# Optimization experiments

Hardware: AMD Instinct MI355X
Metric: run time of the kernel (lower is better)

Reference implementation:

```python
import jax, jax.numpy as jnp
import numpy as np
import math

HIDDEN = 512
NUM_HEADS = 8
HEAD_DIM = HIDDEN // NUM_HEADS  # 64
B, S = 64, 128


def setup_inputs() -> dict:
    key = jax.random.key(0)
    ks = jax.random.split(key, 16)
    sc_h = 1.0 / math.sqrt(HIDDEN)
    sc_d = 1.0 / math.sqrt(HEAD_DIM)
    return {
        "hidden_states": jax.random.normal(ks[0], (B, S, HIDDEN), jnp.float32),
        "attention_mask": jnp.zeros((B, 1, S, S), jnp.float32),
        "structure_matrix": jax.random.normal(ks[1], (B, S, S, HEAD_DIM), jnp.float32),
        # projections stored [in, out]
        "Wq": jax.random.normal(ks[2], (HIDDEN, HIDDEN), jnp.float32) * sc_h,
        "bq": jnp.zeros((HIDDEN,), jnp.float32),
        "Wk": jax.random.normal(ks[3], (HIDDEN, HIDDEN), jnp.float32) * sc_h,
        "bk": jnp.zeros((HIDDEN,), jnp.float32),
        "Wv": jax.random.normal(ks[4], (HIDDEN, HIDDEN), jnp.float32) * sc_h,
        "bv": jnp.zeros((HIDDEN,), jnp.float32),
        "Wsq": jax.random.normal(ks[5], (HEAD_DIM, HEAD_DIM), jnp.float32) * sc_d,
        "bsq": jnp.zeros((HEAD_DIM,), jnp.float32),
        "Wsk": jax.random.normal(ks[6], (HEAD_DIM, HEAD_DIM), jnp.float32) * sc_d,
        "bsk": jnp.zeros((HEAD_DIM,), jnp.float32),
        "Wsv": jax.random.normal(ks[7], (HEAD_DIM, HEAD_DIM), jnp.float32) * sc_d,
        "bsv": jnp.zeros((HEAD_DIM,), jnp.float32),
    }


def _heads(x):
    b, s, _ = x.shape
    return x.reshape(b, s, NUM_HEADS, HEAD_DIM).transpose(0, 2, 1, 3)  # [B,H,S,D]


def reference(hidden_states, attention_mask, structure_matrix,
              Wq, bq, Wk, bk, Wv, bv, Wsq, bsq, Wsk, bsk, Wsv, bsv):
    # projections
    q = _heads(hidden_states @ Wq + bq)  # [B,H,S,D]
    k = _heads(hidden_states @ Wk + bk)
    v = _heads(hidden_states @ Wv + bv)
    sq = structure_matrix @ Wsq + bsq    # [B,S,S,D] (i=key idx, j=query idx)
    sk = structure_matrix @ Wsk + bsk
    sv = structure_matrix @ Wsv + bsv
    # scores[b,h,i,j] = sum_d (k_i + sk_ij)(q_j + sq_ij), expanded to avoid 5D tensor
    scores = (
        jnp.einsum('bhid,bhjd->bhij', k, q)
        + jnp.einsum('bhid,bijd->bhij', k, sq)
        + jnp.einsum('bhjd,bijd->bhij', q, sk)
        + jnp.einsum('bijd,bijd->bij', sk, sq)[:, None]
    ) / math.sqrt(HEAD_DIM)
    scores = scores + attention_mask
    p = jax.nn.relu(scores)
    # note: torch code sums (p + 1e-12) over last dim, i.e. denom = sum(p) + S*1e-12
    p = p / jnp.sum(p + 1e-12, axis=-1, keepdims=True)
    # out[b,h,i,d] = sum_j p_ij * (v_j + sv_ij)
    ctx = (jnp.einsum('bhij,bhjd->bhid', p, v)
           + jnp.einsum('bhij,bijd->bhid', p, sv))
    b = ctx.shape[0]
    return ctx.transpose(0, 2, 1, 3).reshape(b, S, HIDDEN)
```

## Files before the change

kernel.cpp:

```cpp
#include <hip/hip_runtime.h>

#define B_  64
#define S_  128
#define H_  8
#define D_  64
#define HID 512

typedef short short8 __attribute__((ext_vector_type(8)));
typedef float f32x4 __attribute__((ext_vector_type(4)));

__device__ __forceinline__ float bf2f(unsigned short h) {
    union { unsigned int u; float f; } v; v.u = (unsigned int)h << 16; return v.f;
}
__device__ __forceinline__ unsigned short f2bf(float f) {
    union { float f; unsigned int u; } v; v.f = f;
    unsigned int r = v.u + 0x7fffu + ((v.u >> 16) & 1u);
    return (unsigned short)(r >> 16);
}

__global__ __launch_bounds__(256) void wtrans(const float* __restrict__ s0,
                                              const float* __restrict__ s1,
                                              const float* __restrict__ s2,
                                              unsigned short* __restrict__ dst0, int dim)
{
    const float* srcs[3] = {s0, s1, s2};
    const float* src = srcs[blockIdx.z];
    unsigned short* dst = dst0 + (size_t)blockIdx.z * dim * dim;
    __shared__ float tile[32][33];
    const int tx = threadIdx.x & 31, ty = threadIdx.x >> 5;
    const int k0 = blockIdx.x * 32, n0 = blockIdx.y * 32;
    #pragma unroll
    for (int r = 0; r < 4; ++r) {
        int row = ty + r * 8;
        tile[row][tx] = src[(size_t)(k0 + row) * dim + n0 + tx];
    }
    __syncthreads();
    #pragma unroll
    for (int r = 0; r < 4; ++r) {
        int row = ty + r * 8;
        dst[(size_t)(n0 + row) * dim + k0 + tx] = f2bf(tile[tx][row]);
    }
}

__global__ __launch_bounds__(256) void qkv_mfma(
    const float* __restrict__ hidden,
    const unsigned short* __restrict__ wt,
    const float* __restrict__ bq, const float* __restrict__ bk, const float* __restrict__ bv,
    unsigned short* __restrict__ Qb,
    unsigned short* __restrict__ Kb,
    unsigned short* __restrict__ Vb)
{
    const int z = blockIdx.z;
    const unsigned short* W = wt + (size_t)z * HID * HID;
    const float* bias = (z == 0) ? bq : (z == 1) ? bk : bv;
    const int bm = blockIdx.y * 128, bn = blockIdx.x * 128;
    const int t = threadIdx.x, lane = t & 63, w = t >> 6, grp = lane >> 4, l15 = lane & 15;

    __shared__ unsigned short a_s[128 * 72];
    __shared__ unsigned short b_s[128 * 72];

    f32x4 acc[2][8];
    #pragma unroll
    for (int i = 0; i < 2; ++i)
        #pragma unroll
        for (int j = 0; j < 8; ++j) acc[i][j] = (f32x4){0.f, 0.f, 0.f, 0.f};

    for (int k0 = 0; k0 < HID; k0 += 64) {
        #pragma unroll
        for (int it = 0; it < 8; ++it) {
            int idx = t + it * 256;
            int row = idx >> 4, c = idx & 15;
            float4 v4 = *reinterpret_cast<const float4*>(&hidden[(size_t)(bm + row) * HID + k0 + c * 4]);
            ushort4 o = {f2bf(v4.x), f2bf(v4.y), f2bf(v4.z), f2bf(v4.w)};
            *reinterpret_cast<ushort4*>(&a_s[row * 72 + c * 4]) = o;
        }
        #pragma unroll
        for (int it = 0; it < 4; ++it) {
            int idx = t + it * 256;
            int row = idx >> 3, c = idx & 7;
            *reinterpret_cast<short8*>(&b_s[row * 72 + c * 8]) =
                *reinterpret_cast<const short8*>(&W[(size_t)(bn + row) * HID + k0 + c * 8]);
        }
        __syncthreads();
        short8 af[2][2];
        #pragma unroll
        for (int mt = 0; mt < 2; ++mt)
            #pragma unroll
            for (int kk = 0; kk < 2; ++kk)
                af[mt][kk] = *reinterpret_cast<const short8*>(&a_s[(w * 32 + mt * 16 + l15) * 72 + kk * 32 + grp * 8]);
        #pragma unroll
        for (int nt = 0; nt < 8; ++nt) {
            short8 b0 = *reinterpret_cast<const short8*>(&b_s[(nt * 16 + l15) * 72 + grp * 8]);
            short8 b1 = *reinterpret_cast<const short8*>(&b_s[(nt * 16 + l15) * 72 + 32 + grp * 8]);
            #pragma unroll
            for (int mt = 0; mt < 2; ++mt) {
                acc[mt][nt] = __builtin_amdgcn_mfma_f32_16x16x32_bf16(af[mt][0], b0, acc[mt][nt], 0, 0, 0);
                acc[mt][nt] = __builtin_amdgcn_mfma_f32_16x16x32_bf16(af[mt][1], b1, acc[mt][nt], 0, 0, 0);
            }
        }
        __syncthreads();
    }
    unsigned short* dstqk = (z == 0) ? Qb : Kb;
    #pragma unroll
    for (int nt = 0; nt < 8; ++nt) {
        int col = bn + nt * 16 + l15;
        float bval = bias[col];
        #pragma unroll
        for (int mt = 0; mt < 2; ++mt) {
            #pragma unroll
            for (int r = 0; r < 4; ++r) {
                int row = bm + w * 32 + mt * 16 + grp * 4 + r;
                unsigned short val = f2bf(acc[mt][nt][r] + bval);
                if (z == 2) {
                    Vb[(size_t)row * HID + col] = val;
                } else {
                    int bb = row >> 7, jj = row & 127, hh = col >> 6, dd = col & 63;
                    dstqk[(((size_t)bb * H_ + hh) * S_ + jj) * D_ + dd] = val;
                }
            }
        }
    }
}

__global__ __launch_bounds__(256) void kq_gemm(
    const unsigned short* __restrict__ Kb, const unsigned short* __restrict__ Qb,
    float* __restrict__ sc0)
{
    const int bh = blockIdx.x;
    const int t = threadIdx.x, lane = t & 63, w = t >> 6, grp = lane >> 4, l15 = lane & 15;
    const unsigned short* Kp = Kb + (size_t)bh * S_ * D_;
    const unsigned short* Qp = Qb + (size_t)bh * S_ * D_;
    float* outp = sc0 + (size_t)bh * S_ * S_;
    short8 af[2][2];
    #pragma unroll
    for (int mt = 0; mt < 2; ++mt)
        #pragma unroll
        for (int kk = 0; kk < 2; ++kk)
            af[mt][kk] = *reinterpret_cast<const short8*>(&Kp[(size_t)(w * 32 + mt * 16 + l15) * D_ + kk * 32 + grp * 8]);
    #pragma unroll
    for (int nt = 0; nt < 8; ++nt) {
        short8 b0 = *reinterpret_cast<const short8*>(&Qp[(size_t)(nt * 16 + l15) * D_ + grp * 8]);
        short8 b1 = *reinterpret_cast<const short8*>(&Qp[(size_t)(nt * 16 + l15) * D_ + 32 + grp * 8]);
        #pragma unroll
        for (int mt = 0; mt < 2; ++mt) {
            f32x4 a = {0.f, 0.f, 0.f, 0.f};
            a = __builtin_amdgcn_mfma_f32_16x16x32_bf16(af[mt][0], b0, a, 0, 0, 0);
            a = __builtin_amdgcn_mfma_f32_16x16x32_bf16(af[mt][1], b1, a, 0, 0, 0);
            #pragma unroll
            for (int r = 0; r < 4; ++r)
                outp[(size_t)(w * 32 + mt * 16 + grp * 4 + r) * S_ + nt * 16 + l15] = a[r];
        }
    }
}

__global__ __launch_bounds__(256) void attn2(
    const unsigned short* __restrict__ Qb, const unsigned short* __restrict__ Kb,
    const unsigned short* __restrict__ Vb,
    const float* __restrict__ sc0,
    const float* __restrict__ st, const float* __restrict__ mask,
    const unsigned short* __restrict__ wtS,
    const float* __restrict__ bsq, const float* __restrict__ bsk, const float* __restrict__ bsv,
    float* __restrict__ out)
{
    const int i = blockIdx.x, b = blockIdx.y;
    const int t = threadIdx.x, lane = t & 63, w = t >> 6, grp = lane >> 4, l15 = lane & 15;

    __shared__ __align__(16) unsigned char smem[76096];
    unsigned short* st_s = (unsigned short*)smem;
    float*          scf  = (float*)smem;
    unsigned short* sq_s = (unsigned short*)(smem + 18432);
    unsigned short* sk_s = (unsigned short*)(smem + 36864);
    unsigned short* sv_s = (unsigned short*)(smem + 55296);
    unsigned short* k_s  = (unsigned short*)(smem + 73728);
    float*          rsp  = (float*)(smem + 76032);

    {
        const float* stp = st + ((size_t)b * S_ + i) * S_ * D_;
        #pragma unroll
        for (int it = 0; it < 8; ++it) {
            int idx = t + it * 256;
            int row = idx >> 4, c = idx & 15;
            float4 v4 = *reinterpret_cast<const float4*>(stp + (size_t)idx * 4);
            ushort4 o = {f2bf(v4.x), f2bf(v4.y), f2bf(v4.z), f2bf(v4.w)};
            *reinterpret_cast<ushort4*>(&st_s[row * 72 + c * 4]) = o;
        }
        if (t < 64) {
            int h = t >> 3, c = t & 7;
            *reinterpret_cast<short8*>(&k_s[h * 72 + c * 8]) =
                *reinterpret_cast<const short8*>(&Kb[(((size_t)b * H_ + h) * S_ + i) * D_ + c * 8]);
        } else if (t < 128) {
            int h = 8 + ((t - 64) >> 3), c = t & 7;
            short8 zz = {0, 0, 0, 0, 0, 0, 0, 0};
            *reinterpret_cast<short8*>(&k_s[h * 72 + c * 8]) = zz;
        }
    }
    __syncthreads();

    {
        short8 af[2][2];
        #pragma unroll
        for (int mt = 0; mt < 2; ++mt)
            #pragma unroll
            for (int kk = 0; kk < 2; ++kk)
                af[mt][kk] = *reinterpret_cast<const short8*>(&st_s[(w * 32 + mt * 16 + l15) * 72 + kk * 32 + grp * 8]);
        const float* bss[3] = {bsq, bsk, bsv};
        unsigned short* outs[3] = {sq_s, sk_s, sv_s};
        #pragma unroll
        for (int p = 0; p < 3; ++p) {
            const unsigned short* Wp = wtS + (size_t)p * 64 * 64;
            #pragma unroll
            for (int nt = 0; nt < 4; ++nt) {
                short8 b0 = *reinterpret_cast<const short8*>(&Wp[(size_t)(nt * 16 + l15) * 64 + grp * 8]);
                short8 b1 = *reinterpret_cast<const short8*>(&Wp[(size_t)(nt * 16 + l15) * 64 + 32 + grp * 8]);
                float bval = bss[p][nt * 16 + l15];
                #pragma unroll
                for (int mt = 0; mt < 2; ++mt) {
                    f32x4 a = {0.f, 0.f, 0.f, 0.f};
                    a = __builtin_amdgcn_mfma_f32_16x16x32_bf16(af[mt][0], b0, a, 0, 0, 0);
                    a = __builtin_amdgcn_mfma_f32_16x16x32_bf16(af[mt][1], b1, a, 0, 0, 0);
                    #pragma unroll
                    for (int r = 0; r < 4; ++r)
                        outs[p][(w * 32 + mt * 16 + grp * 4 + r) * 72 + nt * 16 + l15] = f2bf(a[r] + bval);
                }
            }
        }
    }
    __syncthreads();

    {
        short8 ka0 = *reinterpret_cast<const short8*>(&k_s[l15 * 72 + grp * 8]);
        short8 ka1 = *reinterpret_cast<const short8*>(&k_s[l15 * 72 + 32 + grp * 8]);
        #pragma unroll
        for (int nt = 0; nt < 2; ++nt) {
            int j0 = w * 32 + nt * 16;
            short8 b0 = *reinterpret_cast<const short8*>(&sq_s[(j0 + l15) * 72 + grp * 8]);
            short8 b1 = *reinterpret_cast<const short8*>(&sq_s[(j0 + l15) * 72 + 32 + grp * 8]);
            f32x4 a = {0.f, 0.f, 0.f, 0.f};
            a = __builtin_amdgcn_mfma_f32_16x16x32_bf16(ka0, b0, a, 0, 0, 0);
            a = __builtin_amdgcn_mfma_f32_16x16x32_bf16(ka1, b1, a, 0, 0, 0);
            if (grp < 2) {
                #pragma unroll
                for (int r = 0; r < 4; ++r)
                    scf[(grp * 4 + r) * 128 + j0 + l15] = a[r];
            }
        }
    }
    __syncthreads();

    const int jj = (w & 1) * 64 + lane;
    const int hg = w >> 1;
    {
        const unsigned short* skr = &sk_s[jj * 72];
        const unsigned short* sqr = &sq_s[jj * 72];
        const unsigned short* qp = Qb + (((size_t)b * H_ + hg * 4) * S_ + jj) * D_;
        float a0 = 0.f, a1 = 0.f, a2 = 0.f, a3 = 0.f, ss = 0.f;
        #pragma unroll
        for (int c = 0; c < 8; ++c) {
            short8 sk8 = *reinterpret_cast<const short8*>(&skr[c * 8]);
            short8 sq8 = *reinterpret_cast<const short8*>(&sqr[c * 8]);
            short8 q0 = *reinterpret_cast<const short8*>(&qp[c * 8]);
            short8 q1 = *reinterpret_cast<const short8*>(&qp[S_ * D_ + c * 8]);
            short8 q2 = *reinterpret_cast<const short8*>(&qp[2 * S_ * D_ + c * 8]);
            short8 q3 = *reinterpret_cast<const short8*>(&qp[3 * S_ * D_ + c * 8]);
            #pragma unroll
            for (int e = 0; e < 8; ++e) {
                float skf = bf2f((unsigned short)sk8[e]);
                float sqf = bf2f((unsigned short)sq8[e]);
                a0 += bf2f((unsigned short)q0[e]) * skf;
                a1 += bf2f((unsigned short)q1[e]) * skf;
                a2 += bf2f((unsigned short)q2[e]) * skf;
                a3 += bf2f((unsigned short)q3[e]) * skf;
                ss += skf * sqf;
            }
        }
        float mv = mask[((size_t)b * S_ + i) * S_ + jj];
        const float* s0p = sc0 + (((size_t)b * H_ + hg * 4) * S_ + i) * S_ + jj;
        float qsk[4] = {a0, a1, a2, a3};
        float pv[4];
        #pragma unroll
        for (int hh = 0; hh < 4; ++hh) {
            int h = hg * 4 + hh;
            float kqv = s0p[(size_t)hh * S_ * S_];
            float ksqv = scf[h * 128 + jj];
            float s = (kqv + ksqv + qsk[hh] + ss) * 0.125f + mv;
            pv[hh] = fmaxf(s, 0.f);
        }
        #pragma unroll
        for (int hh = 0; hh < 4; ++hh) {
            scf[(hg * 4 + hh) * 128 + jj] = pv[hh];
            float r = pv[hh];
            #pragma unroll
            for (int off = 1; off < 64; off <<= 1) r += __shfl_xor(r, off);
            if (lane == 0) rsp[w * 4 + hh] = r;
        }
    }
    __syncthreads();

    {
        const int hc = t >> 6, dc = t & 63;
        const int h0 = hc, h1 = hc + 4;
        float den0 = rsp[((h0 >> 2) * 2) * 4 + (h0 & 3)] + rsp[((h0 >> 2) * 2 + 1) * 4 + (h0 & 3)] + 1.28e-10f;
        float den1 = rsp[((h1 >> 2) * 2) * 4 + (h1 & 3)] + rsp[((h1 >> 2) * 2 + 1) * 4 + (h1 & 3)] + 1.28e-10f;
        const unsigned short* vp = Vb + (size_t)b * S_ * HID;
        float c0 = 0.f, c1 = 0.f;
        #pragma unroll 4
        for (int j = 0; j < S_; ++j) {
            float p0 = scf[h0 * 128 + j];
            float p1 = scf[h1 * 128 + j];
            float svv = bf2f(sv_s[j * 72 + dc]);
            float v0 = bf2f(vp[(size_t)j * HID + h0 * 64 + dc]);
            float v1 = bf2f(vp[(size_t)j * HID + h1 * 64 + dc]);
            c0 += p0 * (v0 + svv);
            c1 += p1 * (v1 + svv);
        }
        float* orow = out + ((size_t)b * S_ + i) * HID;
        orow[t]       = c0 / den0;
        orow[t + 256] = c1 / den1;
    }
}

extern "C" void kernel_launch(void* const* d_in, const int* in_sizes, int n_in,
                              void* d_out, int out_size, void* d_ws, size_t ws_size,
                              hipStream_t stream) {
    const float* hidden = (const float*)d_in[0];
    const float* mask   = (const float*)d_in[1];
    const float* st     = (const float*)d_in[2];
    const float* Wq  = (const float*)d_in[3];
    const float* bq  = (const float*)d_in[4];
    const float* Wk  = (const float*)d_in[5];
    const float* bk  = (const float*)d_in[6];
    const float* Wv  = (const float*)d_in[7];
    const float* bv  = (const float*)d_in[8];
    const float* Wsq = (const float*)d_in[9];
    const float* bsq = (const float*)d_in[10];
    const float* Wsk = (const float*)d_in[11];
    const float* bsk = (const float*)d_in[12];
    const float* Wsv = (const float*)d_in[13];
    const float* bsv = (const float*)d_in[14];
    float* out = (float*)d_out;

    unsigned char* ws = (unsigned char*)d_ws;
    unsigned short* wtB = (unsigned short*)(ws);
    unsigned short* wtS = (unsigned short*)(ws + 1572864);
    unsigned short* Qb  = (unsigned short*)(ws + 1597440);
    unsigned short* Kb  = (unsigned short*)(ws + 9986048);
    unsigned short* Vb  = (unsigned short*)(ws + 18374656);
    float*          sc0 = (float*)(ws + 26763264);

    wtrans<<<dim3(16, 16, 3), 256, 0, stream>>>(Wq, Wk, Wv, wtB, 512);
    wtrans<<<dim3(2, 2, 3), 256, 0, stream>>>(Wsq, Wsk, Wsv, wtS, 64);
    qkv_mfma<<<dim3(4, 64, 3), 256, 0, stream>>>(hidden, wtB, bq, bk, bv, Qb, Kb, Vb);
    kq_gemm<<<dim3(512), 256, 0, stream>>>(Kb, Qb, sc0);
    attn2<<<dim3(S_, B_), 256, 0, stream>>>(Qb, Kb, Vb, sc0, st, mask, wtS, bsq, bsk, bsv, out);
}
```

Before: 470.3 us.

## Rewrite attention kernel with multi-row blocks, prefetch, swizzled LDS and MFMA PV

Replaces the per-row attention kernel with one that processes 8 query rows per block, register-prefetching the next structure-matrix slice while computing the current one. LDS layouts drop padding in favor of XOR swizzles, block indices are remapped for locality, and the P·(V+SV) product moves from scalar loops to MFMA using a transposed V layout emitted by the QKV GEMM. The K·Q scores and probabilities are stored as bf16, and packed hardware bf16 conversion is used. This cuts global traffic and scalar FMA work but lowers precision and serializes 8 rows per block, reducing the number of blocks available for parallelism.

```diff
diff --git a/kernel.cpp b/kernel.cpp
--- a/kernel.cpp
+++ b/kernel.cpp
@@ -5,6 +5,7 @@
 #define H_  8
 #define D_  64
 #define HID 512
+#define G_  8
 
 typedef short short8 __attribute__((ext_vector_type(8)));
 typedef float f32x4 __attribute__((ext_vector_type(4)));
@@ -16,6 +17,11 @@
     union { float f; unsigned int u; } v; v.f = f;
     unsigned int r = v.u + 0x7fffu + ((v.u >> 16) & 1u);
     return (unsigned short)(r >> 16);
+}
+__device__ __forceinline__ unsigned int cvt_pk_bf16(float lo, float hi) {
+    unsigned int r;
+    asm("v_cvt_pk_bf16_f32 %0, %1, %2" : "=v"(r) : "v"(lo), "v"(hi));
+    return r;
 }
 
 __global__ __launch_bounds__(256) void wtrans(const float* __restrict__ s0,
@@ -48,7 +54,7 @@
     const float* __restrict__ bq, const float* __restrict__ bk, const float* __restrict__ bv,
     unsigned short* __restrict__ Qb,
     unsigned short* __restrict__ Kb,
-    unsigned short* __restrict__ Vb)
+    unsigned short* __restrict__ VT)
 {
     const int z = blockIdx.z;
     const unsigned short* W = wt + (size_t)z * HID * HID;
@@ -71,8 +77,9 @@
             int idx = t + it * 256;
             int row = idx >> 4, c = idx & 15;
             float4 v4 = *reinterpret_cast<const float4*>(&hidden[(size_t)(bm + row) * HID + k0 + c * 4]);
-            ushort4 o = {f2bf(v4.x), f2bf(v4.y), f2bf(v4.z), f2bf(v4.w)};
-            *reinterpret_cast<ushort4*>(&a_s[row * 72 + c * 4]) = o;
+            unsigned int lo = cvt_pk_bf16(v4.x, v4.y);
+            unsigned int hi = cvt_pk_bf16(v4.z, v4.w);
+            *reinterpret_cast<uint2*>(&a_s[row * 72 + c * 4]) = make_uint2(lo, hi);
         }
         #pragma unroll
         for (int it = 0; it < 4; ++it) {
@@ -111,10 +118,10 @@
             for (int r = 0; r < 4; ++r) {
                 int row = bm + w * 32 + mt * 16 + grp * 4 + r;
                 unsigned short val = f2bf(acc[mt][nt][r] + bval);
+                int bb = row >> 7, jj = row & 127, hh = col >> 6, dd = col & 63;
                 if (z == 2) {
-                    Vb[(size_t)row * HID + col] = val;
+                    VT[(((size_t)bb * H_ + hh) * D_ + dd) * S_ + jj] = val;
                 } else {
-                    int bb = row >> 7, jj = row & 127, hh = col >> 6, dd = col & 63;
                     dstqk[(((size_t)bb * H_ + hh) * S_ + jj) * D_ + dd] = val;
                 }
             }
@@ -124,13 +131,13 @@
 
 __global__ __launch_bounds__(256) void kq_gemm(
     const unsigned short* __restrict__ Kb, const unsigned short* __restrict__ Qb,
-    float* __restrict__ sc0)
+    unsigned short* __restrict__ sc0)
 {
     const int bh = blockIdx.x;
     const int t = threadIdx.x, lane = t & 63, w = t >> 6, grp = lane >> 4, l15 = lane & 15;
     const unsigned short* Kp = Kb + (size_t)bh * S_ * D_;
     const unsigned short* Qp = Qb + (size_t)bh * S_ * D_;
-    float* outp = sc0 + (size_t)bh * S_ * S_;
+    unsigned short* outp = sc0 + (size_t)bh * S_ * S_;
     short8 af[2][2];
     #pragma unroll
     for (int mt = 0; mt < 2; ++mt)
@@ -148,174 +155,215 @@
             a = __builtin_amdgcn_mfma_f32_16x16x32_bf16(af[mt][1], b1, a, 0, 0, 0);
             #pragma unroll
             for (int r = 0; r < 4; ++r)
-                outp[(size_t)(w * 32 + mt * 16 + grp * 4 + r) * S_ + nt * 16 + l15] = a[r];
-        }
-    }
-}
-
-__global__ __launch_bounds__(256) void attn2(
+                outp[(size_t)(w * 32 + mt * 16 + grp * 4 + r) * S_ + nt * 16 + l15] = f2bf(a[r]);
+        }
+    }
+}
+
+__global__ __launch_bounds__(256) void attn3(
     const unsigned short* __restrict__ Qb, const unsigned short* __restrict__ Kb,
-    const unsigned short* __restrict__ Vb,
-    const float* __restrict__ sc0,
+    const unsigned short* __restrict__ VT,
+    const unsigned short* __restrict__ sc0,
     const float* __restrict__ st, const float* __restrict__ mask,
     const unsigned short* __restrict__ wtS,
     const float* __restrict__ bsq, const float* __restrict__ bsk, const float* __restrict__ bsv,
     float* __restrict__ out)
 {
-    const int i = blockIdx.x, b = blockIdx.y;
+    const int flat = blockIdx.y * gridDim.x + blockIdx.x;
+    const int swz  = (flat & 7) * 128 + (flat >> 3);
+    const int b  = swz >> 4;
+    const int ig = swz & 15;
     const int t = threadIdx.x, lane = t & 63, w = t >> 6, grp = lane >> 4, l15 = lane & 15;
 
-    __shared__ __align__(16) unsigned char smem[76096];
-    unsigned short* st_s = (unsigned short*)smem;
-    float*          scf  = (float*)smem;
-    unsigned short* sq_s = (unsigned short*)(smem + 18432);
-    unsigned short* sk_s = (unsigned short*)(smem + 36864);
-    unsigned short* sv_s = (unsigned short*)(smem + 55296);
-    unsigned short* k_s  = (unsigned short*)(smem + 73728);
-    float*          rsp  = (float*)(smem + 76032);
-
+    __shared__ __align__(16) unsigned char smem[53312];
+    float* rsp = (float*)(smem + 53248);
+
+    const float* stbase = st + (size_t)b * S_ * S_ * D_;
+    float4 stg[8];
     {
-        const float* stp = st + ((size_t)b * S_ + i) * S_ * D_;
-        #pragma unroll
-        for (int it = 0; it < 8; ++it) {
-            int idx = t + it * 256;
-            int row = idx >> 4, c = idx & 15;
-            float4 v4 = *reinterpret_cast<const float4*>(stp + (size_t)idx * 4);
-            ushort4 o = {f2bf(v4.x), f2bf(v4.y), f2bf(v4.z), f2bf(v4.w)};
-            *reinterpret_cast<ushort4*>(&st_s[row * 72 + c * 4]) = o;
+        const float* p = stbase + (size_t)(ig * G_) * (S_ * D_);
+        #pragma unroll
+        for (int l = 0; l < 8; ++l)
+            stg[l] = *reinterpret_cast<const float4*>(p + (size_t)(t + l * 256) * 4);
+    }
+
+    for (int it = 0; it < G_; ++it) {
+        const int i = ig * G_ + it;
+
+        #pragma unroll
+        for (int l = 0; l < 8; ++l) {
+            const int idx = t + l * 256;
+            const int row = idx >> 4, c = idx & 15;
+            unsigned int lo = cvt_pk_bf16(stg[l].x, stg[l].y);
+            unsigned int hi = cvt_pk_bf16(stg[l].z, stg[l].w);
+            *reinterpret_cast<uint2*>((char*)smem + row * 128 + ((((c >> 1) ^ (row & 7)) << 4)) + 8 * (c & 1))
+                = make_uint2(lo, hi);
+        }
+        __syncthreads();
+
+        short8 af[2][2];
+        #pragma unroll
+        for (int mt = 0; mt < 2; ++mt) {
+            const int row = w * 32 + mt * 16 + l15, rs = row & 7;
+            af[mt][0] = *reinterpret_cast<const short8*>((const char*)smem + row * 128 + ((grp ^ rs) << 4));
+            af[mt][1] = *reinterpret_cast<const short8*>((const char*)smem + row * 128 + (((4 + grp) ^ rs) << 4));
+        }
+        __syncthreads();
+
+        if (it + 1 < G_) {
+            const float* nxt = stbase + (size_t)(i + 1) * (S_ * D_);
+            #pragma unroll
+            for (int l = 0; l < 8; ++l)
+                stg[l] = *reinterpret_cast<const float4*>(nxt + (size_t)(t + l * 256) * 4);
         }
         if (t < 64) {
-            int h = t >> 3, c = t & 7;
-            *reinterpret_cast<short8*>(&k_s[h * 72 + c * 8]) =
-                *reinterpret_cast<const short8*>(&Kb[(((size_t)b * H_ + h) * S_ + i) * D_ + c * 8]);
-        } else if (t < 128) {
-            int h = 8 + ((t - 64) >> 3), c = t & 7;
-            short8 zz = {0, 0, 0, 0, 0, 0, 0, 0};
-            *reinterpret_cast<short8*>(&k_s[h * 72 + c * 8]) = zz;
-        }
-    }
-    __syncthreads();
-
-    {
-        short8 af[2][2];
-        #pragma unroll
-        for (int mt = 0; mt < 2; ++mt)
-            #pragma unroll
-            for (int kk = 0; kk < 2; ++kk)
-                af[mt][kk] = *reinterpret_cast<const short8*>(&st_s[(w * 32 + mt * 16 + l15) * 72 + kk * 32 + grp * 8]);
-        const float* bss[3] = {bsq, bsk, bsv};
-        unsigned short* outs[3] = {sq_s, sk_s, sv_s};
-        #pragma unroll
-        for (int p = 0; p < 3; ++p) {
-            const unsigned short* Wp = wtS + (size_t)p * 64 * 64;
-            #pragma unroll
-            for (int nt = 0; nt < 4; ++nt) {
-                short8 b0 = *reinterpret_cast<const short8*>(&Wp[(size_t)(nt * 16 + l15) * 64 + grp * 8]);
-                short8 b1 = *reinterpret_cast<const short8*>(&Wp[(size_t)(nt * 16 + l15) * 64 + 32 + grp * 8]);
-                float bval = bss[p][nt * 16 + l15];
+            const int h = t >> 3, c = t & 7;
+            short8 kv = *reinterpret_cast<const short8*>(&Kb[(((size_t)b * H_ + h) * S_ + i) * D_ + c * 8]);
+            *reinterpret_cast<short8*>((char*)smem + 49152 + h * 128 + (((c ^ (h & 7)) << 4))) = kv;
+        }
+        {
+            #pragma unroll
+            for (int p = 0; p < 3; ++p) {
+                const unsigned short* Wp = wtS + p * (D_ * D_);
+                const float* bsp = (p == 0) ? bsq : (p == 1) ? bsk : bsv;
                 #pragma unroll
-                for (int mt = 0; mt < 2; ++mt) {
-                    f32x4 a = {0.f, 0.f, 0.f, 0.f};
-                    a = __builtin_amdgcn_mfma_f32_16x16x32_bf16(af[mt][0], b0, a, 0, 0, 0);
-                    a = __builtin_amdgcn_mfma_f32_16x16x32_bf16(af[mt][1], b1, a, 0, 0, 0);
+                for (int nt = 0; nt < 4; ++nt) {
+                    short8 bf0 = *reinterpret_cast<const short8*>(&Wp[(size_t)(nt * 16 + l15) * D_ + grp * 8]);
+                    short8 bf1 = *reinterpret_cast<const short8*>(&Wp[(size_t)(nt * 16 + l15) * D_ + 32 + grp * 8]);
+                    float bval = bsp[nt * 16 + l15];
+                    #pragma unroll
+                    for (int mt = 0; mt < 2; ++mt) {
+                        f32x4 a = (f32x4){0.f, 0.f, 0.f, 0.f};
+                        a = __builtin_amdgcn_mfma_f32_16x16x32_bf16(af[mt][0], bf0, a, 0, 0, 0);
+                        a = __builtin_amdgcn_mfma_f32_16x16x32_bf16(af[mt][1], bf1, a, 0, 0, 0);
+                        const int jrow = w * 32 + mt * 16 + grp * 4;
+                        if (p == 2) {
+                            const int e = nt * 16 + l15;
+                            unsigned int lo = cvt_pk_bf16(a[0] + bval, a[1] + bval);
+                            unsigned int hi = cvt_pk_bf16(a[2] + bval, a[3] + bval);
+                            const int slot = (4 * w + 2 * mt + (grp >> 1)) ^ (e & 7);
+                            *reinterpret_cast<uint2*>((char*)smem + 32768 + (e << 8) + (slot << 4) + 8 * (grp & 1))
+                                = make_uint2(lo, hi);
+                        } else {
+                            char* oB = (char*)smem + (p == 0 ? 16384 : 0);
+                            #pragma unroll
+                            for (int r = 0; r < 4; ++r) {
+                                const int row = jrow + r;
+                                const int slot = (2 * nt + (l15 >> 3)) ^ (row & 7);
+                                *reinterpret_cast<unsigned short*>(oB + row * 128 + (slot << 4) + ((2 * l15) & 15))
+                                    = f2bf(a[r] + bval);
+                            }
+                        }
+                    }
+                }
+            }
+        }
+        __syncthreads();
+
+        {
+            const char* kB = (const char*)smem + 49152;
+            const int ks = l15 & 7;
+            short8 ka0 = *reinterpret_cast<const short8*>(kB + l15 * 128 + ((grp ^ ks) << 4));
+            short8 ka1 = *reinterpret_cast<const short8*>(kB + l15 * 128 + (((4 + grp) ^ ks) << 4));
+            unsigned short* kqs = (unsigned short*)(smem + 51200);
+            const char* sqB = (const char*)smem + 16384;
+            #pragma unroll
+            for (int nt2 = 0; nt2 < 2; ++nt2) {
+                const int j0 = w * 32 + nt2 * 16;
+                const int row = j0 + l15, rs = row & 7;
+                short8 b0 = *reinterpret_cast<const short8*>(sqB + row * 128 + ((grp ^ rs) << 4));
+                short8 b1 = *reinterpret_cast<const short8*>(sqB + row * 128 + (((4 + grp) ^ rs) << 4));
+                f32x4 a = (f32x4){0.f, 0.f, 0.f, 0.f};
+                a = __builtin_amdgcn_mfma_f32_16x16x32_bf16(ka0, b0, a, 0, 0, 0);
+                a = __builtin_amdgcn_mfma_f32_16x16x32_bf16(ka1, b1, a, 0, 0, 0);
+                if (grp < 2) {
                     #pragma unroll
                     for (int r = 0; r < 4; ++r)
-                        outs[p][(w * 32 + mt * 16 + grp * 4 + r) * 72 + nt * 16 + l15] = f2bf(a[r] + bval);
+                        kqs[(grp * 4 + r) * S_ + j0 + l15] = f2bf(a[r]);
                 }
             }
         }
-    }
-    __syncthreads();
-
-    {
-        short8 ka0 = *reinterpret_cast<const short8*>(&k_s[l15 * 72 + grp * 8]);
-        short8 ka1 = *reinterpret_cast<const short8*>(&k_s[l15 * 72 + 32 + grp * 8]);
-        #pragma unroll
-        for (int nt = 0; nt < 2; ++nt) {
-            int j0 = w * 32 + nt * 16;
-            short8 b0 = *reinterpret_cast<const short8*>(&sq_s[(j0 + l15) * 72 + grp * 8]);
-            short8 b1 = *reinterpret_cast<const short8*>(&sq_s[(j0 + l15) * 72 + 32 + grp * 8]);
-            f32x4 a = {0.f, 0.f, 0.f, 0.f};
-            a = __builtin_amdgcn_mfma_f32_16x16x32_bf16(ka0, b0, a, 0, 0, 0);
-            a = __builtin_amdgcn_mfma_f32_16x16x32_bf16(ka1, b1, a, 0, 0, 0);
-            if (grp < 2) {
+        __syncthreads();
+
+        {
+            const int jj = (w & 1) * 64 + lane;
+            const int hg = w >> 1;
+            const int jsw = jj & 7;
+            const char* skB = (const char*)smem + jj * 128;
+            const char* sqB = (const char*)smem + 16384 + jj * 128;
+            const unsigned short* qp = Qb + (((size_t)b * H_ + hg * 4) * S_ + jj) * D_;
+            float a0 = 0.f, a1 = 0.f, a2 = 0.f, a3 = 0.f, ss = 0.f;
+            #pragma unroll
+            for (int c = 0; c < 8; ++c) {
+                const int off = (c ^ jsw) << 4;
+                short8 sk8 = *reinterpret_cast<const short8*>(skB + off);
+                short8 sq8 = *reinterpret_cast<const short8*>(sqB + off);
+                short8 q0 = *reinterpret_cast<const short8*>(&qp[c * 8]);
+                short8 q1 = *reinterpret_cast<const short8*>(&qp[S_ * D_ + c * 8]);
+                short8 q2 = *reinterpret_cast<const short8*>(&qp[2 * S_ * D_ + c * 8]);
+                short8 q3 = *reinterpret_cast<const short8*>(&qp[3 * S_ * D_ + c * 8]);
                 #pragma unroll
-                for (int r = 0; r < 4; ++r)
-                    scf[(grp * 4 + r) * 128 + j0 + l15] = a[r];
-            }
-        }
-    }
-    __syncthreads();
-
-    const int jj = (w & 1) * 64 + lane;
-    const int hg = w >> 1;
-    {
-        const unsigned short* skr = &sk_s[jj * 72];
-        const unsigned short* sqr = &sq_s[jj * 72];
-        const unsigned short* qp = Qb + (((size_t)b * H_ + hg * 4) * S_ + jj) * D_;
-        float a0 = 0.f, a1 = 0.f, a2 = 0.f, a3 = 0.f, ss = 0.f;
-        #pragma unroll
-        for (int c = 0; c < 8; ++c) {
-            short8 sk8 = *reinterpret_cast<const short8*>(&skr[c * 8]);
-            short8 sq8 = *reinterpret_cast<const short8*>(&sqr[c * 8]);
-            short8 q0 = *reinterpret_cast<const short8*>(&qp[c * 8]);
-            short8 q1 = *reinterpret_cast<const short8*>(&qp[S_ * D_ + c * 8]);
-            short8 q2 = *reinterpret_cast<const short8*>(&qp[2 * S_ * D_ + c * 8]);
-            short8 q3 = *reinterpret_cast<const short8*>(&qp[3 * S_ * D_ + c * 8]);
-            #pragma unroll
-            for (int e = 0; e < 8; ++e) {
-                float skf = bf2f((unsigned short)sk8[e]);
-                float sqf = bf2f((unsigned short)sq8[e]);
-                a0 += bf2f((unsigned short)q0[e]) * skf;
-                a1 += bf2f((unsigned short)q1[e]) * skf;
-                a2 += bf2f((unsigned short)q2[e]) * skf;
-                a3 += bf2f((unsigned short)q3[e]) * skf;
-                ss += skf * sqf;
-            }
-        }
-        float mv = mask[((size_t)b * S_ + i) * S_ + jj];
-        const float* s0p = sc0 + (((size_t)b * H_ + hg * 4) * S_ + i) * S_ + jj;
-        float qsk[4] = {a0, a1, a2, a3};
-        float pv[4];
-        #pragma unroll
-        for (int hh = 0; hh < 4; ++hh) {
-            int h = hg * 4 + hh;
-            float kqv = s0p[(size_t)hh * S_ * S_];
-            float ksqv = scf[h * 128 + jj];
-            float s = (kqv + ksqv + qsk[hh] + ss) * 0.125f + mv;
-            pv[hh] = fmaxf(s, 0.f);
-        }
-        #pragma unroll
-        for (int hh = 0; hh < 4; ++hh) {
-            scf[(hg * 4 + hh) * 128 + jj] = pv[hh];
-            float r = pv[hh];
-            #pragma unroll
-            for (int off = 1; off < 64; off <<= 1) r += __shfl_xor(r, off);
-            if (lane == 0) rsp[w * 4 + hh] = r;
-        }
-    }
-    __syncthreads();
-
-    {
-        const int hc = t >> 6, dc = t & 63;
-        const int h0 = hc, h1 = hc + 4;
-        float den0 = rsp[((h0 >> 2) * 2) * 4 + (h0 & 3)] + rsp[((h0 >> 2) * 2 + 1) * 4 + (h0 & 3)] + 1.28e-10f;
-        float den1 = rsp[((h1 >> 2) * 2) * 4 + (h1 & 3)] + rsp[((h1 >> 2) * 2 + 1) * 4 + (h1 & 3)] + 1.28e-10f;
-        const unsigned short* vp = Vb + (size_t)b * S_ * HID;
-        float c0 = 0.f, c1 = 0.f;
-        #pragma unroll 4
-        for (int j = 0; j < S_; ++j) {
-            float p0 = scf[h0 * 128 + j];
-            float p1 = scf[h1 * 128 + j];
-            float svv = bf2f(sv_s[j * 72 + dc]);
-            float v0 = bf2f(vp[(size_t)j * HID + h0 * 64 + dc]);
-            float v1 = bf2f(vp[(size_t)j * HID + h1 * 64 + dc]);
-            c0 += p0 * (v0 + svv);
-            c1 += p1 * (v1 + svv);
-        }
-        float* orow = out + ((size_t)b * S_ + i) * HID;
-        orow[t]       = c0 / den0;
-        orow[t + 256] = c1 / den1;
+                for (int e = 0; e < 8; ++e) {
+                    float skf = bf2f((unsigned short)sk8[e]);
+                    float sqf = bf2f((unsigned short)sq8[e]);
+                    a0 += bf2f((unsigned short)q0[e]) * skf;
+                    a1 += bf2f((unsigned short)q1[e]) * skf;
+                    a2 += bf2f((unsigned short)q2[e]) * skf;
+                    a3 += bf2f((unsigned short)q3[e]) * skf;
+                    ss += skf * sqf;
+                }
+            }
+            const float mv = mask[((size_t)b * S_ + i) * S_ + jj];
+            const unsigned short* s0p = sc0 + (((size_t)b * H_ + hg * 4) * S_ + i) * S_ + jj;
+            const unsigned short* kqs = (const unsigned short*)(smem + 51200);
+            unsigned short* pbf = (unsigned short*)(smem + 49152);
+            float qsk[4] = {a0, a1, a2, a3};
+            #pragma unroll
+            for (int hh = 0; hh < 4; ++hh) {
+                const int h = hg * 4 + hh;
+                float kqv  = bf2f(s0p[(size_t)hh * S_ * S_]);
+                float ksqv = bf2f(kqs[h * S_ + jj]);
+                float s = (kqv + ksqv + qsk[hh] + ss) * 0.125f + mv;
+                float pv = fmaxf(s, 0.f);
+                pbf[h * S_ + jj] = f2bf(pv);
+                float r = pv;
+                #pragma unroll
+                for (int o2 = 1; o2 < 64; o2 <<= 1) r += __shfl_xor(r, o2);
+                if (lane == 0) rsp[w * 4 + hh] = r;
+            }
+        }
+        __syncthreads();
+
+        {
+            #pragma unroll
+            for (int hh = 0; hh < 2; ++hh) {
+                const int h = w + hh * 4;
+                const unsigned short* pb = (const unsigned short*)(smem + 49152) + h * S_;
+                short8 pa[4];
+                #pragma unroll
+                for (int kk = 0; kk < 4; ++kk)
+                    pa[kk] = *reinterpret_cast<const short8*>(&pb[kk * 32 + grp * 8]);
+                const float den = rsp[hh * 8 + w] + rsp[hh * 8 + 4 + w] + 1.28e-10f;
+                const float inv = 1.0f / den;
+                const unsigned short* vtb = VT + ((size_t)b * H_ + h) * (D_ * S_);
+                #pragma unroll
+                for (int nt = 0; nt < 4; ++nt) {
+                    const int e = nt * 16 + l15, es = e & 7;
+                    const char* svRow = (const char*)smem + 32768 + (e << 8);
+                    f32x4 a = (f32x4){0.f, 0.f, 0.f, 0.f};
+                    #pragma unroll
+                    for (int kk = 0; kk < 4; ++kk)
+                        a = __builtin_amdgcn_mfma_f32_16x16x32_bf16(
+                            pa[kk], *reinterpret_cast<const short8*>(&vtb[(size_t)e * S_ + kk * 32 + grp * 8]), a, 0, 0, 0);
+                    #pragma unroll
+                    for (int kk = 0; kk < 4; ++kk)
+                        a = __builtin_amdgcn_mfma_f32_16x16x32_bf16(
+                            pa[kk], *reinterpret_cast<const short8*>(svRow + (((4 * kk + grp) ^ es) << 4)), a, 0, 0, 0);
+                    if (grp == 0)
+                        out[((size_t)b * S_ + i) * HID + h * D_ + nt * 16 + l15] = a[0] * inv;
+                }
+            }
+        }
     }
 }
 
@@ -344,12 +392,12 @@
     unsigned short* wtS = (unsigned short*)(ws + 1572864);
     unsigned short* Qb  = (unsigned short*)(ws + 1597440);
     unsigned short* Kb  = (unsigned short*)(ws + 9986048);
-    unsigned short* Vb  = (unsigned short*)(ws + 18374656);
-    float*          sc0 = (float*)(ws + 26763264);
+    unsigned short* VT  = (unsigned short*)(ws + 18374656);
+    unsigned short* sc0 = (unsigned short*)(ws + 26763264);
 
     wtrans<<<dim3(16, 16, 3), 256, 0, stream>>>(Wq, Wk, Wv, wtB, 512);
     wtrans<<<dim3(2, 2, 3), 256, 0, stream>>>(Wsq, Wsk, Wsv, wtS, 64);
-    qkv_mfma<<<dim3(4, 64, 3), 256, 0, stream>>>(hidden, wtB, bq, bk, bv, Qb, Kb, Vb);
+    qkv_mfma<<<dim3(4, 64, 3), 256, 0, stream>>>(hidden, wtB, bq, bk, bv, Qb, Kb, VT);
     kq_gemm<<<dim3(512), 256, 0, stream>>>(Kb, Qb, sc0);
-    attn2<<<dim3(S_, B_), 256, 0, stream>>>(Qb, Kb, Vb, sc0, st, mask, wtS, bsq, bsk, bsv, out);
-}
+    attn3<<<dim3(16, 64), 256, 0, stream>>>(Qb, Kb, VT, sc0, st, mask, wtS, bsq, bsk, bsv, out);
+}
```

Measured after the change: 613.5 us. +30.4%, slower.
